# Kernel optimization log

Hardware: AMD Instinct MI355X
Metric: run time of the kernel (lower is better)

The kernel has to match this reference:

```python
import jax, jax.numpy as jnp
import numpy as np

B, N, L, D, H = 2, 2048, 2048, 1024, 16
HD = D // H  # 64


def setup_inputs() -> dict:
    key = jax.random.key(0)
    ks = jax.random.split(key, 12)
    s = 0.02
    return {
        "x_q": jax.random.normal(ks[0], (B, N, D), jnp.float32),
        "x_kv": jax.random.normal(ks[1], (B, L, D), jnp.float32),
        "pad_mask": jax.random.randint(ks[2], (B, L), 0, 2) > 0,
        "wq": jax.random.normal(ks[3], (D, D), jnp.float32) * s,
        "bq": jnp.zeros((D,), jnp.float32),
        "wk": jax.random.normal(ks[4], (D, D), jnp.float32) * s,
        "bk": jnp.zeros((D,), jnp.float32),
        "wv": jax.random.normal(ks[5], (D, D), jnp.float32) * s,
        "bv": jnp.zeros((D,), jnp.float32),
        "wo": jax.random.normal(ks[6], (D, D), jnp.float32) * s,
        "bo": jnp.zeros((D,), jnp.float32),
    }


def reference(x_q, x_kv, pad_mask, wq, bq, wk, bk, wv, bv, wo, bo):
    scale = HD ** -0.5
    # projections: (B, S, D) -> (B, H, S, HD)
    def split_heads(x):
        return x.reshape(x.shape[0], x.shape[1], H, HD).transpose(0, 2, 1, 3)
    q = split_heads(x_q @ wq + bq) * scale
    k = split_heads(x_kv @ wk + bk)
    v = split_heads(x_kv @ wv + bv)
    attn = jnp.einsum('bhic,bhjc->bhij', q, k)  # (B, H, N, L)
    neg = -jnp.finfo(attn.dtype).max
    attn = jnp.where(pad_mask[:, None, None, :], neg, attn)
    attn = jax.nn.softmax(attn, axis=-1)
    o = jnp.einsum('bhij,bhjc->bhic', attn, v)  # (B, H, N, HD)
    o = o.transpose(0, 2, 1, 3).reshape(B, N, D)
    return o @ wo + bo
```

## Files before the change

### kernel.cpp

```cpp
#include <hip/hip_runtime.h>
#include <hip/hip_bf16.h>
#include <math.h>

typedef __bf16 bf16;
typedef __attribute__((ext_vector_type(8))) __bf16 bf16x8;
typedef __attribute__((ext_vector_type(4))) __bf16 bf16x4;
typedef __attribute__((ext_vector_type(4))) float floatx4;
typedef __attribute__((ext_vector_type(16))) float floatx16;

#define BB 2
#define NN 2048
#define LL 2048
#define DD 1024
#define HH 16
#define HDD 64

#define QSCALE (0.125f * 1.44269504f)
#define PCLAMP 21.66f
#define MBIAS  (-100000.0f)

__device__ __forceinline__ void async16(const bf16* g, bf16* l) {
  __builtin_amdgcn_global_load_lds((const __attribute__((address_space(1))) void*)(g),
                                   (__attribute__((address_space(3))) void*)(l), 16, 0, 0);
}

__device__ __forceinline__ unsigned cvtpk(float a, float b) {
  unsigned r;
  asm("v_cvt_pk_bf16_f32 %0, %1, %2" : "=v"(r) : "v"(a), "v"(b));
  return r;
}

__device__ __forceinline__ void plswap(unsigned &x, unsigned &y) {
  auto r = __builtin_amdgcn_permlane32_swap(x, y, false, false);
  x = (unsigned)r[0];
  y = (unsigned)r[1];
}

__device__ __forceinline__ bf16x8 mk_frag(unsigned w0, unsigned w1, unsigned w2, unsigned w3) {
  union { unsigned u[4]; bf16x8 b; } f;
  f.u[0] = w0; f.u[1] = w1; f.u[2] = w2; f.u[3] = w3;
  return f.b;
}

__global__ __launch_bounds__(256) void prep_kernel(
    const float* __restrict__ xq, const float* __restrict__ xkv,
    bf16* __restrict__ Xqb, bf16* __restrict__ Xkvb, int nconv, int elemsEach,
    const float* __restrict__ W0, const float* __restrict__ W1,
    const float* __restrict__ W2, const float* __restrict__ W3,
    bf16* __restrict__ T0, bf16* __restrict__ T1,
    bf16* __restrict__ T2, bf16* __restrict__ T3,
    const unsigned* __restrict__ mask, float* __restrict__ biasF)
{
  __shared__ bf16 Tb[64][72];
  const int bid = blockIdx.x;
  const int t = threadIdx.x;

  if (bid < nconv) {
    const int half = nconv >> 1;
    const float* s = (bid < half) ? xq : xkv;
    bf16* d = (bid < half) ? Xqb : Xkvb;
    int gid = (bid < half) ? bid : bid - half;
    int idx = (gid * 256 + t) * 8;
    if (idx >= elemsEach) return;
    floatx4 a = *(const floatx4*)&s[idx];
    floatx4 b = *(const floatx4*)&s[idx + 4];
    bf16x8 o;
#pragma unroll
    for (int e = 0; e < 4; e++) { o[e] = (bf16)a[e]; o[4 + e] = (bf16)b[e]; }
    *(bf16x8*)&d[idx] = o;
    return;
  }
  if (bid < nconv + 1024) {
    const int wb = bid - nconv;
    const int which = wb >> 8;
    const float* W = which == 0 ? W0 : which == 1 ? W1 : which == 2 ? W2 : W3;
    bf16*       T = which == 0 ? T0 : which == 1 ? T1 : which == 2 ? T2 : T3;
    const int tile = wb & 255;
    const int k0 = (tile >> 4) * 64, n0 = (tile & 15) * 64;
    const int r = t >> 2;
    const int c = (t & 3) * 16;
    const float* Wr = W + (size_t)(k0 + r) * 1024 + n0 + c;
    floatx4 f0 = *(const floatx4*)(Wr + 0);
    floatx4 f1 = *(const floatx4*)(Wr + 4);
    floatx4 f2 = *(const floatx4*)(Wr + 8);
    floatx4 f3 = *(const floatx4*)(Wr + 12);
#pragma unroll
    for (int e = 0; e < 4; e++) {
      Tb[c + e][r]      = (bf16)f0[e];
      Tb[c + 4 + e][r]  = (bf16)f1[e];
      Tb[c + 8 + e][r]  = (bf16)f2[e];
      Tb[c + 12 + e][r] = (bf16)f3[e];
    }
    __syncthreads();
    bf16* Tr = T + (size_t)(n0 + r) * 1024 + k0 + c;
    *(bf16x8*)&Tr[0] = *(const bf16x8*)&Tb[r][c];
    *(bf16x8*)&Tr[8] = *(const bf16x8*)&Tb[r][c + 8];
    return;
  }
  __shared__ int hasBig, hasFloat;
  if (t == 0) { hasBig = 0; hasFloat = 0; }
  __syncthreads();
  int big = 0, flt = 0;
  for (int idx = t; idx < 1024; idx += 256) {
    unsigned v = mask[idx];
    if (v == 0x3F800000u) flt = 1;
    else if (v > 1u) big = 1;
  }
  if (big) atomicOr(&hasBig, 1);
  if (flt) atomicOr(&hasFloat, 1);
  __syncthreads();
  const int mode = hasFloat ? 2 : (hasBig ? 1 : 0);
  for (int k = t * 16; k < t * 16 + 16; k++) {
    bool m;
    if (mode == 0)      m = ((const int*)mask)[k] != 0;
    else if (mode == 1) m = ((const unsigned char*)mask)[k] != 0;
    else                m = ((const float*)mask)[k] != 0.0f;
    biasF[k] = m ? MBIAS : 0.0f;
  }
}

template <typename TC>
__device__ __forceinline__ void gemm_body32(
    int bx, const bf16* __restrict__ A, const bf16* __restrict__ Wt,
    const float* __restrict__ bias, TC* __restrict__ C, float scale, int transv)
{
  __shared__ bf16 As[3][128 * 32];
  __shared__ bf16 Bs[3][128 * 32];

  const int tm = bx >> 3, tn = bx & 7;
  const int m0 = tm * 128, n0 = tn * 128;
  const int t = threadIdx.x;
  const int w = t >> 6, l = t & 63;
  const int col = l & 31, half = l >> 5;
  const int wm = (w >> 1) * 64, wn = (w & 1) * 64;
  const int sr  = t >> 2;
  const int scl = (t & 3) * 8;
  const int scs = (((t & 3) ^ ((t >> 3) & 3)) * 8);
  const int csw = (col >> 1) & 3;

  floatx16 acc[2][2];
#pragma unroll
  for (int mi = 0; mi < 2; mi++)
#pragma unroll
    for (int ni = 0; ni < 2; ni++)
#pragma unroll
      for (int e = 0; e < 16; e++) acc[mi][ni][e] = 0.0f;

  auto STAGE = [&](int k0, int s) {
    async16(&A[(size_t)(m0 + sr) * 1024 + k0 + scs],       &As[s][sr * 32 + scl]);
    async16(&A[(size_t)(m0 + 64 + sr) * 1024 + k0 + scs],  &As[s][(64 + sr) * 32 + scl]);
    async16(&Wt[(size_t)(n0 + sr) * 1024 + k0 + scs],      &Bs[s][sr * 32 + scl]);
    async16(&Wt[(size_t)(n0 + 64 + sr) * 1024 + k0 + scs], &Bs[s][(64 + sr) * 32 + scl]);
  };

  STAGE(0, 0);
  const int NK = 1024 / 32;
  for (int k = 0; k < NK; k++) {
    if (k + 1 < NK) {
      STAGE((k + 1) * 32, (k + 1) % 3);
      asm volatile("s_waitcnt vmcnt(4)" ::: "memory");
    } else {
      asm volatile("s_waitcnt vmcnt(0)" ::: "memory");
    }
    __builtin_amdgcn_s_barrier();
    __builtin_amdgcn_sched_barrier(0);
    const bf16* as = &As[k % 3][0];
    const bf16* bs = &Bs[k % 3][0];
#pragma unroll
    for (int kk = 0; kk < 2; kk++) {
      const int ch = ((kk * 2 + half) ^ csw) * 8;
      bf16x8 af[2], bfr[2];
#pragma unroll
      for (int mi = 0; mi < 2; mi++)
        af[mi] = *(const bf16x8*)&as[(wm + mi * 32 + col) * 32 + ch];
#pragma unroll
      for (int ni = 0; ni < 2; ni++)
        bfr[ni] = *(const bf16x8*)&bs[(wn + ni * 32 + col) * 32 + ch];
#pragma unroll
      for (int mi = 0; mi < 2; mi++)
#pragma unroll
        for (int ni = 0; ni < 2; ni++)
          acc[mi][ni] = __builtin_amdgcn_mfma_f32_32x32x16_bf16(af[mi], bfr[ni], acc[mi][ni], 0, 0, 0);
    }
  }
#pragma unroll
  for (int ni = 0; ni < 2; ni++) {
    int colg = n0 + wn + ni * 32 + col;
    float bv = bias[colg];
#pragma unroll
    for (int mi = 0; mi < 2; mi++) {
      int rbase = m0 + wm + mi * 32 + half * 4;
      if (transv) {
#pragma unroll
        for (int g = 0; g < 4; g++) {
          int key0 = rbase + g * 8;
          int bb = key0 >> 11, key = key0 & 2047;
          bf16x4 v4;
#pragma unroll
          for (int r = 0; r < 4; r++) v4[r] = (bf16)(acc[mi][ni][g * 4 + r] + bv);
          *(bf16x4*)&((bf16*)C)[(size_t)bb * (DD * (size_t)LL) + (size_t)colg * LL + key] = v4;
        }
      } else {
#pragma unroll
        for (int g = 0; g < 4; g++)
#pragma unroll
          for (int r = 0; r < 4; r++)
            C[(size_t)(rbase + g * 8 + r) * 1024 + colg] = (TC)((acc[mi][ni][g * 4 + r] + bv) * scale);
      }
    }
  }
}

__global__ __launch_bounds__(256) void qkv_gemm32(
    const bf16* __restrict__ Xq, const bf16* __restrict__ Xkv,
    const bf16* __restrict__ Wtq, const bf16* __restrict__ Wtk, const bf16* __restrict__ Wtv,
    const float* __restrict__ bq, const float* __restrict__ bk, const float* __restrict__ bv,
    bf16* __restrict__ Qp, bf16* __restrict__ Kp, bf16* __restrict__ VtG, int shift)
{
  const int bid = blockIdx.x;
  const int which = bid >> shift;
  const int bx0 = bid & ((1 << shift) - 1);
  const int q = (1 << shift) >> 3;
  const int bx = (bx0 & 7) * q + (bx0 >> 3);
  if (which == 0)      gemm_body32<bf16>(bx, Xq,  Wtq, bq, Qp,  QSCALE, 0);
  else if (which == 1) gemm_body32<bf16>(bx, Xkv, Wtk, bk, Kp,  1.0f,   0);
  else                 gemm_body32<bf16>(bx, Xkv, Wtv, bv, VtG, 1.0f,   1);
}

__global__ __launch_bounds__(256) void out_gemm(
    const bf16* __restrict__ A, const bf16* __restrict__ Wt,
    const float* __restrict__ bias, float* __restrict__ C)
{
  __shared__ bf16 As[3][128 * 32];
  __shared__ bf16 Bs[3][64 * 32];

  const int bid = blockIdx.x;
  const int qs = gridDim.x >> 3;
  const int bx = (bid & 7) * qs + (bid >> 3);
  const int tm = bx >> 4, tn = bx & 15;
  const int m0 = tm * 128, n0 = tn * 64;
  const int t = threadIdx.x;
  const int w = t >> 6, l = t & 63;
  const int q = l >> 4, i = l & 15;
  const int wm = (w >> 1) * 64, wn = (w & 1) * 32;
  const int sr  = t >> 2;
  const int scl = (t & 3) * 8;
  const int scs = (((t & 3) ^ ((t >> 3) & 3)) * 8);
  const int isw = (i >> 1) & 3;

  const floatx4 zero = {0.f, 0.f, 0.f, 0.f};
  floatx4 acc[4][2];
#pragma unroll
  for (int mi = 0; mi < 4; mi++)
#pragma unroll
    for (int ni = 0; ni < 2; ni++) acc[mi][ni] = zero;

  auto STAGE = [&](int k0, int s) {
    async16(&A[(size_t)(m0 + sr) * 1024 + k0 + scs],       &As[s][sr * 32 + scl]);
    async16(&A[(size_t)(m0 + 64 + sr) * 1024 + k0 + scs],  &As[s][(64 + sr) * 32 + scl]);
    async16(&Wt[(size_t)(n0 + sr) * 1024 + k0 + scs],      &Bs[s][sr * 32 + scl]);
  };

  STAGE(0, 0);
  const int NK = 1024 / 32;
  for (int k = 0; k < NK; k++) {
    if (k + 1 < NK) {
      STAGE((k + 1) * 32, (k + 1) % 3);
      asm volatile("s_waitcnt vmcnt(3)" ::: "memory");
    } else {
      asm volatile("s_waitcnt vmcnt(0)" ::: "memory");
    }
    __builtin_amdgcn_s_barrier();
    __builtin_amdgcn_sched_barrier(0);
    const bf16* as = &As[k % 3][0];
    const bf16* bs = &Bs[k % 3][0];
    const int ch = (q ^ isw) * 8;
    bf16x8 af[4], bfr[2];
#pragma unroll
    for (int mi = 0; mi < 4; mi++)
      af[mi] = *(const bf16x8*)&as[(wm + mi * 16 + i) * 32 + ch];
#pragma unroll
    for (int ni = 0; ni < 2; ni++)
      bfr[ni] = *(const bf16x8*)&bs[(wn + ni * 16 + i) * 32 + ch];
#pragma unroll
    for (int mi = 0; mi < 4; mi++)
#pragma unroll
      for (int ni = 0; ni < 2; ni++)
        acc[mi][ni] = __builtin_amdgcn_mfma_f32_16x16x32_bf16(af[mi], bfr[ni], acc[mi][ni], 0, 0, 0);
  }
#pragma unroll
  for (int ni = 0; ni < 2; ni++) {
    int colg = n0 + wn + ni * 16 + i;
    float bv = bias[colg];
#pragma unroll
    for (int mi = 0; mi < 4; mi++) {
      int row = m0 + wm + mi * 16 + q * 4;
#pragma unroll
      for (int r = 0; r < 4; r++)
        C[(size_t)(row + r) * 1024 + colg] = acc[mi][ni][r] + bv;
    }
  }
}

__global__ __launch_bounds__(256) void attn_kernel(
    const bf16* __restrict__ Q, const bf16* __restrict__ K,
    const bf16* __restrict__ Vt, const float* __restrict__ biasF,
    bf16* __restrict__ O, int hbits)
{
  __shared__ bf16 Kbuf[4][64 * 64];
  __shared__ bf16 Vbuf[4][64 * 64];

  const int bid = blockIdx.x;
  const int qt = bid >> hbits;
  const int hb = bid & ((1 << hbits) - 1);
  const int h  = (hbits == 5) ? (hb >> 1) : hb;
  const int b  = (hbits == 5) ? (hb & 1) : 0;
  const int t = threadIdx.x;
  const int w = t >> 6, lane = t & 63;
  const int col = lane & 31;
  const int hi  = lane >> 5;
  const int lsw = lane & 7;

  const bf16* Qb = Q  + (size_t)b * (NN * DD) + h * HDD;
  const bf16* Kb = K  + (size_t)b * (LL * DD) + h * HDD;
  const bf16* Vb = Vt + (size_t)b * (DD * (size_t)LL) + (size_t)(h * HDD) * LL;
  const float* biasFb = biasF + b * LL;

  const int qrow = qt * 128 + w * 32;

  bf16x8 qfrag[4];
#pragma unroll
  for (int dc = 0; dc < 4; dc++)
    qfrag[dc] = *(const bf16x8*)&Qb[(size_t)(qrow + col) * DD + dc * 16 + hi * 8];

  floatx16 oacc[2];
#pragma unroll
  for (int db = 0; db < 2; db++)
#pragma unroll
    for (int e = 0; e < 16; e++) oacc[db][e] = 0.0f;
  float psum = 0.0f;

  const int sr  = t >> 3;
  const int scl = (t & 7) * 8;
  const int scs = ((t & 7) ^ (sr & 7)) * 8;

  auto STAGE = [&](int tile, int slot) {
    const int k0 = tile * 64;
    async16(&Kb[(size_t)(k0 + sr) * DD + scs],        &Kbuf[slot][sr * 64 + scl]);
    async16(&Kb[(size_t)(k0 + sr + 32) * DD + scs],   &Kbuf[slot][(sr + 32) * 64 + scl]);
    async16(&Vb[(size_t)sr * LL + k0 + scs],          &Vbuf[slot][sr * 64 + scl]);
    async16(&Vb[(size_t)(sr + 32) * LL + k0 + scs],   &Vbuf[slot][(sr + 32) * 64 + scl]);
  };

  floatx4 pb[2][4];
  bf16x8 pfp[4];
  floatx16 sacc[2];

  auto QK = [&](int slot) {
#pragma unroll
    for (int kb = 0; kb < 2; kb++)
#pragma unroll
      for (int g = 0; g < 4; g++)
#pragma unroll
        for (int rr = 0; rr < 4; rr++)
          sacc[kb][g * 4 + rr] = pb[kb][g][rr];
    __builtin_amdgcn_s_setprio(1);
#pragma unroll
    for (int kb = 0; kb < 2; kb++)
#pragma unroll
      for (int dc = 0; dc < 4; dc++) {
        bf16x8 kf = *(const bf16x8*)&Kbuf[slot][(kb * 32 + col) * 64 + ((dc * 2 + hi) ^ lsw) * 8];
        sacc[kb] = __builtin_amdgcn_mfma_f32_32x32x16_bf16(kf, qfrag[dc], sacc[kb], 0, 0, 0);
      }
  };

  auto PV = [&](int slot) {
#pragma unroll
    for (int db = 0; db < 2; db++)
#pragma unroll
      for (int kc = 0; kc < 4; kc++) {
        bf16x8 vf = *(const bf16x8*)&Vbuf[slot][(db * 32 + col) * 64 + ((kc * 2 + hi) ^ lsw) * 8];
        oacc[db] = __builtin_amdgcn_mfma_f32_32x32x16_bf16(vf, pfp[kc], oacc[db], 0, 0, 0);
      }
    __builtin_amdgcn_s_setprio(0);
  };

  auto SOFTMAX = [&](int nextTile) {
#pragma unroll
    for (int kb = 0; kb < 2; kb++)
#pragma unroll
      for (int hh = 0; hh < 2; hh++) {
        float pv[8];
#pragma unroll
        for (int e = 0; e < 8; e++) {
          float p = __builtin_amdgcn_exp2f(fminf(sacc[kb][hh * 8 + e], PCLAMP));
          psum += p;
          pv[e] = p;
        }
        unsigned a0 = cvtpk(pv[0], pv[1]);
        unsigned a1 = cvtpk(pv[2], pv[3]);
        unsigned b0 = cvtpk(pv[4], pv[5]);
        unsigned b1 = cvtpk(pv[6], pv[7]);
        plswap(a0, b0);
        plswap(a1, b1);
        pfp[kb * 2 + hh] = mk_frag(a0, a1, b0, b1);
      }
    const int kn = (nextTile & 31) * 64;
#pragma unroll
    for (int kb = 0; kb < 2; kb++)
#pragma unroll
      for (int g = 0; g < 4; g++)
        pb[kb][g] = *(const floatx4*)&biasFb[kn + kb * 32 + g * 8 + hi * 4];
  };

#pragma unroll
  for (int kb = 0; kb < 2; kb++)
#pragma unroll
    for (int g = 0; g < 4; g++)
      pb[kb][g] = *(const floatx4*)&biasFb[kb * 32 + g * 8 + hi * 4];
  STAGE(0, 0);
  STAGE(1, 1);

  asm volatile("s_waitcnt vmcnt(4)" ::: "memory");
  __builtin_amdgcn_s_barrier();
  __builtin_amdgcn_sched_barrier(0);

  QK(0);
  __builtin_amdgcn_s_setprio(0);
  SOFTMAX(1);

  const int NT = LL / 64;
  for (int kt = 1; kt < NT; kt++) {
    if (kt + 1 < NT) {
      STAGE(kt + 1, (kt + 1) & 3);
      asm volatile("s_waitcnt vmcnt(4)" ::: "memory");
    } else {
      asm volatile("s_waitcnt vmcnt(0)" ::: "memory");
    }
    __builtin_amdgcn_s_barrier();
    __builtin_amdgcn_sched_barrier(0);
    QK(kt & 3);
    PV((kt - 1) & 3);
    SOFTMAX(kt + 1);
  }
  __builtin_amdgcn_s_setprio(1);
  PV((NT - 1) & 3);

  psum += __shfl_xor(psum, 32, 64);
  float inv = 1.0f / fmaxf(psum, 1e-30f);

  bf16* Ob = O + (size_t)b * (NN * DD) + h * HDD;
#pragma unroll
  for (int db = 0; db < 2; db++)
#pragma unroll
    for (int g = 0; g < 4; g++) {
      bf16x4 v4;
#pragma unroll
      for (int rr = 0; rr < 4; rr++) v4[rr] = (bf16)(oacc[db][g * 4 + rr] * inv);
      *(bf16x4*)&Ob[(size_t)(qrow + col) * DD + db * 32 + g * 8 + hi * 4] = v4;
    }
}

extern "C" void kernel_launch(void* const* d_in, const int* in_sizes, int n_in,
                              void* d_out, int out_size, void* d_ws, size_t ws_size,
                              hipStream_t stream)
{
  const float* x_q  = (const float*)d_in[0];
  const float* x_kv = (const float*)d_in[1];
  const void*  pad  = d_in[2];
  const float* wq = (const float*)d_in[3];
  const float* bq = (const float*)d_in[4];
  const float* wk = (const float*)d_in[5];
  const float* bk = (const float*)d_in[6];
  const float* wv = (const float*)d_in[7];
  const float* bv = (const float*)d_in[8];
  const float* wo = (const float*)d_in[9];
  const float* bo = (const float*)d_in[10];
  float* out = (float*)d_out;

  char* ws = (char*)d_ws;
  const size_t MB = (size_t)1 << 20;
  const size_t fullElems = (size_t)BB * NN * DD;
  const size_t batchElems = (size_t)NN * DD;

  if (ws_size >= 49 * MB) {
    bf16* Xqb   = (bf16*)(ws);
    bf16* Xkvb  = (bf16*)(ws + 8 * MB);
    bf16* Wtq   = (bf16*)(ws + 16 * MB);
    bf16* Wtk   = (bf16*)(ws + 18 * MB);
    bf16* Wtv   = (bf16*)(ws + 20 * MB);
    bf16* Wto   = (bf16*)(ws + 22 * MB);
    bf16* Qp    = (bf16*)(ws + 24 * MB);
    bf16* Kp    = (bf16*)(ws + 32 * MB);
    bf16* VtG   = (bf16*)(ws + 40 * MB);
    float* biasF = (float*)(ws + 48 * MB);
    bf16* Op    = Xqb;

    prep_kernel<<<5121, 256, 0, stream>>>(x_q, x_kv, Xqb, Xkvb, 4096, (int)fullElems,
                                          wq, wk, wv, wo, Wtq, Wtk, Wtv, Wto,
                                          (const unsigned*)pad, biasF);
    qkv_gemm32<<<768, 256, 0, stream>>>(Xqb, Xkvb, Wtq, Wtk, Wtv, bq, bk, bv, Qp, Kp, VtG, 8);
    attn_kernel<<<512, 256, 0, stream>>>(Qp, Kp, VtG, biasF, Op, 5);
    out_gemm<<<512, 256, 0, stream>>>(Op, Wto, bo, out);
  } else {
    bf16* Wtq   = (bf16*)(ws);
    bf16* Wtk   = (bf16*)(ws + 2 * MB);
    bf16* Wtv   = (bf16*)(ws + 4 * MB);
    bf16* Wto   = (bf16*)(ws + 6 * MB);
    bf16* Xqb   = (bf16*)(ws + 8 * MB);
    bf16* Xkvb  = (bf16*)(ws + 12 * MB);
    bf16* Qp    = (bf16*)(ws + 16 * MB);
    bf16* Kp    = (bf16*)(ws + 20 * MB);
    bf16* VtG   = (bf16*)(ws + 24 * MB);
    float* biasF = (float*)(ws + 28 * MB);
    bf16* Op    = Xqb;

    for (int b = 0; b < BB; b++) {
      if (b == 0)
        prep_kernel<<<3073, 256, 0, stream>>>(x_q, x_kv, Xqb, Xkvb, 2048, (int)batchElems,
                                              wq, wk, wv, wo, Wtq, Wtk, Wtv, Wto,
                                              (const unsigned*)pad, biasF);
      else
        prep_kernel<<<2048, 256, 0, stream>>>(x_q + b * batchElems, x_kv + b * batchElems,
                                              Xqb, Xkvb, 2048, (int)batchElems,
                                              wq, wk, wv, wo, Wtq, Wtk, Wtv, Wto,
                                              (const unsigned*)pad, biasF);
      qkv_gemm32<<<384, 256, 0, stream>>>(Xqb, Xkvb, Wtq, Wtk, Wtv, bq, bk, bv, Qp, Kp, VtG, 7);
      attn_kernel<<<256, 256, 0, stream>>>(Qp, Kp, VtG, biasF + b * LL, Op, 4);
      out_gemm<<<256, 256, 0, stream>>>(Op, Wto, bo, out + b * batchElems);
    }
  }
}
```

Measured before the change: 217.3 us.

## Deepen GEMM prefetch to four LDS stages and split QKV launch into three

```diff
diff --git a/kernel.cpp b/kernel.cpp
--- a/kernel.cpp
+++ b/kernel.cpp
@@ -124,8 +124,8 @@
     int bx, const bf16* __restrict__ A, const bf16* __restrict__ Wt,
     const float* __restrict__ bias, TC* __restrict__ C, float scale, int transv)
 {
-  __shared__ bf16 As[3][128 * 32];
-  __shared__ bf16 Bs[3][128 * 32];
+  __shared__ bf16 As[4][128 * 32];
+  __shared__ bf16 Bs[4][128 * 32];
 
   const int tm = bx >> 3, tn = bx & 7;
   const int m0 = tm * 128, n0 = tn * 128;
@@ -154,18 +154,19 @@
   };
 
   STAGE(0, 0);
+  STAGE(32, 1);
+  STAGE(64, 2);
   const int NK = 1024 / 32;
   for (int k = 0; k < NK; k++) {
-    if (k + 1 < NK) {
-      STAGE((k + 1) * 32, (k + 1) % 3);
-      asm volatile("s_waitcnt vmcnt(4)" ::: "memory");
-    } else {
-      asm volatile("s_waitcnt vmcnt(0)" ::: "memory");
-    }
+    if (k + 3 <= NK - 1)      asm volatile("s_waitcnt vmcnt(8)" ::: "memory");
+    else if (k + 2 <= NK - 1) asm volatile("s_waitcnt vmcnt(8)" ::: "memory");
+    else if (k + 1 <= NK - 1) asm volatile("s_waitcnt vmcnt(4)" ::: "memory");
+    else                      asm volatile("s_waitcnt vmcnt(0)" ::: "memory");
     __builtin_amdgcn_s_barrier();
     __builtin_amdgcn_sched_barrier(0);
-    const bf16* as = &As[k % 3][0];
-    const bf16* bs = &Bs[k % 3][0];
+    if (k + 3 < NK) STAGE((k + 3) * 32, (k + 3) & 3);
+    const bf16* as = &As[k & 3][0];
+    const bf16* bs = &Bs[k & 3][0];
 #pragma unroll
     for (int kk = 0; kk < 2; kk++) {
       const int ch = ((kk * 2 + half) ^ csw) * 8;
@@ -215,13 +216,11 @@
     const bf16* __restrict__ Xq, const bf16* __restrict__ Xkv,
     const bf16* __restrict__ Wtq, const bf16* __restrict__ Wtk, const bf16* __restrict__ Wtv,
     const float* __restrict__ bq, const float* __restrict__ bk, const float* __restrict__ bv,
-    bf16* __restrict__ Qp, bf16* __restrict__ Kp, bf16* __restrict__ VtG, int shift)
+    bf16* __restrict__ Qp, bf16* __restrict__ Kp, bf16* __restrict__ VtG, int shift, int which)
 {
   const int bid = blockIdx.x;
-  const int which = bid >> shift;
-  const int bx0 = bid & ((1 << shift) - 1);
   const int q = (1 << shift) >> 3;
-  const int bx = (bx0 & 7) * q + (bx0 >> 3);
+  const int bx = (bid & 7) * q + (bid >> 3);
   if (which == 0)      gemm_body32<bf16>(bx, Xq,  Wtq, bq, Qp,  QSCALE, 0);
   else if (which == 1) gemm_body32<bf16>(bx, Xkv, Wtk, bk, Kp,  1.0f,   0);
   else                 gemm_body32<bf16>(bx, Xkv, Wtv, bv, VtG, 1.0f,   1);
@@ -231,8 +230,8 @@
     const bf16* __restrict__ A, const bf16* __restrict__ Wt,
     const float* __restrict__ bias, float* __restrict__ C)
 {
-  __shared__ bf16 As[3][128 * 32];
-  __shared__ bf16 Bs[3][64 * 32];
+  __shared__ bf16 As[4][128 * 32];
+  __shared__ bf16 Bs[4][64 * 32];
 
   const int bid = blockIdx.x;
   const int qs = gridDim.x >> 3;
@@ -262,18 +261,18 @@
   };
 
   STAGE(0, 0);
+  STAGE(32, 1);
+  STAGE(64, 2);
   const int NK = 1024 / 32;
   for (int k = 0; k < NK; k++) {
-    if (k + 1 < NK) {
-      STAGE((k + 1) * 32, (k + 1) % 3);
-      asm volatile("s_waitcnt vmcnt(3)" ::: "memory");
-    } else {
-      asm volatile("s_waitcnt vmcnt(0)" ::: "memory");
-    }
+    if (k + 2 <= NK - 1)      asm volatile("s_waitcnt vmcnt(6)" ::: "memory");
+    else if (k + 1 <= NK - 1) asm volatile("s_waitcnt vmcnt(3)" ::: "memory");
+    else                      asm volatile("s_waitcnt vmcnt(0)" ::: "memory");
     __builtin_amdgcn_s_barrier();
     __builtin_amdgcn_sched_barrier(0);
-    const bf16* as = &As[k % 3][0];
-    const bf16* bs = &Bs[k % 3][0];
+    if (k + 3 < NK) STAGE((k + 3) * 32, (k + 3) & 3);
+    const bf16* as = &As[k & 3][0];
+    const bf16* bs = &Bs[k & 3][0];
     const int ch = (q ^ isw) * 8;
     bf16x8 af[4], bfr[2];
 #pragma unroll
@@ -499,7 +498,9 @@
     prep_kernel<<<5121, 256, 0, stream>>>(x_q, x_kv, Xqb, Xkvb, 4096, (int)fullElems,
                                           wq, wk, wv, wo, Wtq, Wtk, Wtv, Wto,
                                           (const unsigned*)pad, biasF);
-    qkv_gemm32<<<768, 256, 0, stream>>>(Xqb, Xkvb, Wtq, Wtk, Wtv, bq, bk, bv, Qp, Kp, VtG, 8);
+    qkv_gemm32<<<256, 256, 0, stream>>>(Xqb, Xkvb, Wtq, Wtk, Wtv, bq, bk, bv, Qp, Kp, VtG, 8, 1);
+    qkv_gemm32<<<256, 256, 0, stream>>>(Xqb, Xkvb, Wtq, Wtk, Wtv, bq, bk, bv, Qp, Kp, VtG, 8, 2);
+    qkv_gemm32<<<256, 256, 0, stream>>>(Xqb, Xkvb, Wtq, Wtk, Wtv, bq, bk, bv, Qp, Kp, VtG, 8, 0);
     attn_kernel<<<512, 256, 0, stream>>>(Qp, Kp, VtG, biasF, Op, 5);
     out_gemm<<<512, 256, 0, stream>>>(Op, Wto, bo, out);
   } else {
@@ -525,7 +526,9 @@
                                               Xqb, Xkvb, 2048, (int)batchElems,
                                               wq, wk, wv, wo, Wtq, Wtk, Wtv, Wto,
                                               (const unsigned*)pad, biasF);
-      qkv_gemm32<<<384, 256, 0, stream>>>(Xqb, Xkvb, Wtq, Wtk, Wtv, bq, bk, bv, Qp, Kp, VtG, 7);
+      qkv_gemm32<<<128, 256, 0, stream>>>(Xqb, Xkvb, Wtq, Wtk, Wtv, bq, bk, bv, Qp, Kp, VtG, 7, 1);
+      qkv_gemm32<<<128, 256, 0, stream>>>(Xqb, Xkvb, Wtq, Wtk, Wtv, bq, bk, bv, Qp, Kp, VtG, 7, 2);
+      qkv_gemm32<<<128, 256, 0, stream>>>(Xqb, Xkvb, Wtq, Wtk, Wtv, bq, bk, bv, Qp, Kp, VtG, 7, 0);
       attn_kernel<<<256, 256, 0, stream>>>(Qp, Kp, VtG, biasF + b * LL, Op, 4);
       out_gemm<<<256, 256, 0, stream>>>(Op, Wto, bo, out + b * batchElems);
     }
```

Measured after the change: 246.5 us. 1.13x slower.

## Split attention KV range across two wave groups per block with LDS reduction

Applied to the files above, without the earlier changes.

```diff
diff --git a/kernel.cpp b/kernel.cpp
--- a/kernel.cpp
+++ b/kernel.cpp
@@ -302,13 +302,14 @@
   }
 }
 
-__global__ __launch_bounds__(256) void attn_kernel(
+__global__ __launch_bounds__(512, 4) void attn_kernel(
     const bf16* __restrict__ Q, const bf16* __restrict__ K,
     const bf16* __restrict__ Vt, const float* __restrict__ biasF,
     bf16* __restrict__ O, int hbits)
 {
-  __shared__ bf16 Kbuf[4][64 * 64];
-  __shared__ bf16 Vbuf[4][64 * 64];
+  __shared__ __align__(16) char smem[73728];
+  bf16* KVl = (bf16*)smem;
+  float* biasLds = (float*)(smem + 65536);
 
   const int bid = blockIdx.x;
   const int qt = bid >> hbits;
@@ -317,6 +318,8 @@
   const int b  = (hbits == 5) ? (hb & 1) : 0;
   const int t = threadIdx.x;
   const int w = t >> 6, lane = t & 63;
+  const int kg = w >> 2;
+  const int wi = w & 3;
   const int col = lane & 31;
   const int hi  = lane >> 5;
   const int lsw = lane & 7;
@@ -326,7 +329,7 @@
   const bf16* Vb = Vt + (size_t)b * (DD * (size_t)LL) + (size_t)(h * HDD) * LL;
   const float* biasFb = biasF + b * LL;
 
-  const int qrow = qt * 128 + w * 32;
+  const int qrow = qt * 128 + wi * 32;
 
   bf16x8 qfrag[4];
 #pragma unroll
@@ -340,52 +343,57 @@
     for (int e = 0; e < 16; e++) oacc[db][e] = 0.0f;
   float psum = 0.0f;
 
-  const int sr  = t >> 3;
-  const int scl = (t & 7) * 8;
-  const int scs = ((t & 7) ^ (sr & 7)) * 8;
+  *(floatx4*)&biasLds[t * 4] = *(const floatx4*)&biasFb[t * 4];
+
+  const int tl  = t & 255;
+  const int sr  = tl >> 3;
+  const int scl = (tl & 7) * 8;
+  const int scs = ((tl & 7) ^ (sr & 7)) * 8;
 
   auto STAGE = [&](int tile, int slot) {
     const int k0 = tile * 64;
-    async16(&Kb[(size_t)(k0 + sr) * DD + scs],        &Kbuf[slot][sr * 64 + scl]);
-    async16(&Kb[(size_t)(k0 + sr + 32) * DD + scs],   &Kbuf[slot][(sr + 32) * 64 + scl]);
-    async16(&Vb[(size_t)sr * LL + k0 + scs],          &Vbuf[slot][sr * 64 + scl]);
-    async16(&Vb[(size_t)(sr + 32) * LL + k0 + scs],   &Vbuf[slot][(sr + 32) * 64 + scl]);
+    bf16* Kd = KVl + (kg * 2 + slot) * 4096;
+    bf16* Vd = KVl + 16384 + (kg * 2 + slot) * 4096;
+    async16(&Kb[(size_t)(k0 + sr) * DD + scs],      Kd + sr * 64 + scl);
+    async16(&Kb[(size_t)(k0 + sr + 32) * DD + scs], Kd + (sr + 32) * 64 + scl);
+    async16(&Vb[(size_t)sr * LL + k0 + scs],        Vd + sr * 64 + scl);
+    async16(&Vb[(size_t)(sr + 32) * LL + k0 + scs], Vd + (sr + 32) * 64 + scl);
   };
 
-  floatx4 pb[2][4];
+  STAGE(kg * 16, 0);
+
   bf16x8 pfp[4];
   floatx16 sacc[2];
 
-  auto QK = [&](int slot) {
+  const int NTg = 16;
+  for (int i = 0; i < NTg; i++) {
+    const int T = kg * 16 + i;
+    const int slot = i & 1;
+    __syncthreads();
+    if (i + 1 < NTg) STAGE(T + 1, (i + 1) & 1);
+
+    const bf16* Kc = KVl + (kg * 2 + slot) * 4096;
+    const bf16* Vc = KVl + 16384 + (kg * 2 + slot) * 4096;
+
+    const int kn = T * 64;
 #pragma unroll
     for (int kb = 0; kb < 2; kb++)
 #pragma unroll
-      for (int g = 0; g < 4; g++)
-#pragma unroll
-        for (int rr = 0; rr < 4; rr++)
-          sacc[kb][g * 4 + rr] = pb[kb][g][rr];
+      for (int gg = 0; gg < 4; gg++) {
+        floatx4 pbv = *(const floatx4*)&biasLds[kn + kb * 32 + gg * 8 + hi * 4];
+#pragma unroll
+        for (int rr = 0; rr < 4; rr++) sacc[kb][gg * 4 + rr] = pbv[rr];
+      }
     __builtin_amdgcn_s_setprio(1);
 #pragma unroll
     for (int kb = 0; kb < 2; kb++)
 #pragma unroll
       for (int dc = 0; dc < 4; dc++) {
-        bf16x8 kf = *(const bf16x8*)&Kbuf[slot][(kb * 32 + col) * 64 + ((dc * 2 + hi) ^ lsw) * 8];
+        bf16x8 kf = *(const bf16x8*)&Kc[(kb * 32 + col) * 64 + ((dc * 2 + hi) ^ lsw) * 8];
         sacc[kb] = __builtin_amdgcn_mfma_f32_32x32x16_bf16(kf, qfrag[dc], sacc[kb], 0, 0, 0);
       }
-  };
-
-  auto PV = [&](int slot) {
-#pragma unroll
-    for (int db = 0; db < 2; db++)
-#pragma unroll
-      for (int kc = 0; kc < 4; kc++) {
-        bf16x8 vf = *(const bf16x8*)&Vbuf[slot][(db * 32 + col) * 64 + ((kc * 2 + hi) ^ lsw) * 8];
-        oacc[db] = __builtin_amdgcn_mfma_f32_32x32x16_bf16(vf, pfp[kc], oacc[db], 0, 0, 0);
-      }
     __builtin_amdgcn_s_setprio(0);
-  };
-
-  auto SOFTMAX = [&](int nextTile) {
+
 #pragma unroll
     for (int kb = 0; kb < 2; kb++)
 #pragma unroll
@@ -405,60 +413,53 @@
         plswap(a1, b1);
         pfp[kb * 2 + hh] = mk_frag(a0, a1, b0, b1);
       }
-    const int kn = (nextTile & 31) * 64;
-#pragma unroll
-    for (int kb = 0; kb < 2; kb++)
-#pragma unroll
-      for (int g = 0; g < 4; g++)
-        pb[kb][g] = *(const floatx4*)&biasFb[kn + kb * 32 + g * 8 + hi * 4];
-  };
-
-#pragma unroll
-  for (int kb = 0; kb < 2; kb++)
-#pragma unroll
-    for (int g = 0; g < 4; g++)
-      pb[kb][g] = *(const floatx4*)&biasFb[kb * 32 + g * 8 + hi * 4];
-  STAGE(0, 0);
-  STAGE(1, 1);
-
-  asm volatile("s_waitcnt vmcnt(4)" ::: "memory");
-  __builtin_amdgcn_s_barrier();
-  __builtin_amdgcn_sched_barrier(0);
-
-  QK(0);
-  __builtin_amdgcn_s_setprio(0);
-  SOFTMAX(1);
-
-  const int NT = LL / 64;
-  for (int kt = 1; kt < NT; kt++) {
-    if (kt + 1 < NT) {
-      STAGE(kt + 1, (kt + 1) & 3);
-      asm volatile("s_waitcnt vmcnt(4)" ::: "memory");
-    } else {
-      asm volatile("s_waitcnt vmcnt(0)" ::: "memory");
-    }
-    __builtin_amdgcn_s_barrier();
-    __builtin_amdgcn_sched_barrier(0);
-    QK(kt & 3);
-    PV((kt - 1) & 3);
-    SOFTMAX(kt + 1);
-  }
-  __builtin_amdgcn_s_setprio(1);
-  PV((NT - 1) & 3);
-
-  psum += __shfl_xor(psum, 32, 64);
-  float inv = 1.0f / fmaxf(psum, 1e-30f);
-
-  bf16* Ob = O + (size_t)b * (NN * DD) + h * HDD;
-#pragma unroll
-  for (int db = 0; db < 2; db++)
-#pragma unroll
-    for (int g = 0; g < 4; g++) {
-      bf16x4 v4;
-#pragma unroll
-      for (int rr = 0; rr < 4; rr++) v4[rr] = (bf16)(oacc[db][g * 4 + rr] * inv);
-      *(bf16x4*)&Ob[(size_t)(qrow + col) * DD + db * 32 + g * 8 + hi * 4] = v4;
-    }
+
+    __builtin_amdgcn_s_setprio(1);
+#pragma unroll
+    for (int db = 0; db < 2; db++)
+#pragma unroll
+      for (int kc = 0; kc < 4; kc++) {
+        bf16x8 vf = *(const bf16x8*)&Vc[(db * 32 + col) * 64 + ((kc * 2 + hi) ^ lsw) * 8];
+        oacc[db] = __builtin_amdgcn_mfma_f32_32x32x16_bf16(vf, pfp[kc], oacc[db], 0, 0, 0);
+      }
+    __builtin_amdgcn_s_setprio(0);
+  }
+
+  __syncthreads();
+  float* sOacc = (float*)smem;
+  float* sPsum = (float*)(smem + 4 * 64 * 33 * 4);
+  if (kg == 1) {
+    const int base = (wi * 64 + lane) * 33;
+#pragma unroll
+    for (int db = 0; db < 2; db++)
+#pragma unroll
+      for (int e = 0; e < 16; e++)
+        sOacc[base + db * 16 + e] = oacc[db][e];
+    sPsum[wi * 64 + lane] = psum;
+  }
+  __syncthreads();
+  if (kg == 0) {
+    const int base = (wi * 64 + lane) * 33;
+#pragma unroll
+    for (int db = 0; db < 2; db++)
+#pragma unroll
+      for (int e = 0; e < 16; e++)
+        oacc[db][e] += sOacc[base + db * 16 + e];
+    psum += sPsum[wi * 64 + lane];
+    psum += __shfl_xor(psum, 32, 64);
+    float inv = 1.0f / fmaxf(psum, 1e-30f);
+
+    bf16* Ob = O + (size_t)b * (NN * DD) + h * HDD;
+#pragma unroll
+    for (int db = 0; db < 2; db++)
+#pragma unroll
+      for (int gg = 0; gg < 4; gg++) {
+        bf16x4 v4;
+#pragma unroll
+        for (int rr = 0; rr < 4; rr++) v4[rr] = (bf16)(oacc[db][gg * 4 + rr] * inv);
+        *(bf16x4*)&Ob[(size_t)(qrow + col) * DD + db * 32 + gg * 8 + hi * 4] = v4;
+      }
+  }
 }
 
 extern "C" void kernel_launch(void* const* d_in, const int* in_sizes, int n_in,
@@ -500,7 +501,7 @@
                                           wq, wk, wv, wo, Wtq, Wtk, Wtv, Wto,
                                           (const unsigned*)pad, biasF);
     qkv_gemm32<<<768, 256, 0, stream>>>(Xqb, Xkvb, Wtq, Wtk, Wtv, bq, bk, bv, Qp, Kp, VtG, 8);
-    attn_kernel<<<512, 256, 0, stream>>>(Qp, Kp, VtG, biasF, Op, 5);
+    attn_kernel<<<512, 512, 0, stream>>>(Qp, Kp, VtG, biasF, Op, 5);
     out_gemm<<<512, 256, 0, stream>>>(Op, Wto, bo, out);
   } else {
     bf16* Wtq   = (bf16*)(ws);
@@ -526,7 +527,7 @@
                                               wq, wk, wv, wo, Wtq, Wtk, Wtv, Wto,
                                               (const unsigned*)pad, biasF);
       qkv_gemm32<<<384, 256, 0, stream>>>(Xqb, Xkvb, Wtq, Wtk, Wtv, bq, bk, bv, Qp, Kp, VtG, 7);
-      attn_kernel<<<256, 256, 0, stream>>>(Qp, Kp, VtG, biasF + b * LL, Op, 4);
+      attn_kernel<<<256, 512, 0, stream>>>(Qp, Kp, VtG, biasF + b * LL, Op, 4);
       out_gemm<<<256, 256, 0, stream>>>(Op, Wto, bo, out + b * batchElems);
     }
   }
```

After: 209.3 us, median of 4. 3.7% less time.
